# Performance work log

Measured on AMD Instinct MI355X. Metric: run time of the kernel, lower is better.

Reference implementation:

```python
import jax, jax.numpy as jnp
import numpy as np

B, N, RBF, F = 4, 512, 32, 16
EPS = 1e-7


def _levi_civita():
    e = np.zeros((3, 3, 3), np.float32)
    e[0, 1, 2] = e[1, 2, 0] = e[2, 0, 1] = 1.0
    e[0, 2, 1] = e[2, 1, 0] = e[1, 0, 2] = -1.0
    return jnp.asarray(e)


def setup_inputs() -> dict:
    key = jax.random.key(0)
    ks = jax.random.split(key, 8)
    g = lambda k, s, sc=1.0: jax.random.normal(k, s, dtype=jnp.float32) * sc
    w_sc = RBF ** -0.5
    return dict(
        image=jax.random.uniform(ks[0], (B, N, N, RBF), dtype=jnp.float32),
        vectors=g(ks[1], (B, N, N, 3)),
        feat0=g(ks[2], (B, N, F, 1)),
        feat1=g(ks[3], (B, N, F, 3)),
        W00=g(ks[4], (RBF, F), w_sc), b00=jnp.zeros((F,), jnp.float32),
        W01=g(ks[5], (RBF, F), w_sc), b01=jnp.zeros((F,), jnp.float32),
        W10=g(ks[6], (RBF, F), w_sc), b10=jnp.zeros((F,), jnp.float32),
        W11=g(ks[7], (RBF, F), w_sc), b11=jnp.zeros((F,), jnp.float32),
    )


def _masked(radial, vectors):
    # zero the radial where the pair vector has (near) zero norm (self-pairs)
    keep = jnp.linalg.norm(vectors, axis=-1) >= EPS  # (B,N,N)
    return jnp.where(keep[..., None], radial, jnp.zeros_like(radial))


def reference(image, vectors, feat0, feat1, W00, b00, W01, b01, W10, b10, W11, b11):
    # radial networks: Dense(rbf -> F), one per (input tensor, filter order)
    r00 = image @ W00 + b00                      # (B,N,N,F) RO0 filter for RO0 input
    r01 = _masked(image @ W01 + b01, vectors)    # RO1 filter for RO0 input
    r10 = image @ W10 + b10                      # RO0 filter for RO1 input
    r11 = _masked(image @ W11 + b11, vectors)    # RO1 filter for RO1 input

    f0 = feat0[..., 0]                           # (B,N,F)
    # Note: RO1 filter F1[m,a,b,f,j] = vectors[m,a,b,j] * masked_radial[m,a,b,f];
    # fused into the einsums to avoid materializing (B,N,N,F,3).
    out1 = jnp.einsum('mabf,mbf->maf', r00, f0)[..., None]                 # 0x0->0
    out2 = jnp.einsum('mabi,mabf,mbf->mafi', vectors, r01, f0)             # 1x0->1
    out3 = jnp.einsum('mabf,mbfi->mafi', r10, feat1)                       # 0x1->1
    out4 = jnp.einsum('mabj,mabf,mbfj->maf', vectors, r11, feat1)[..., None]  # 1x1->0
    e = _levi_civita()
    out5 = jnp.einsum('ijk,mabj,mabf,mbfk->mafi', e, vectors, r11, feat1)  # 1x1->1
    return (out1, out2, out3, out4, out5)
```

## Files before the change

### kernel.cpp

```cpp
#include <hip/hip_runtime.h>


typedef __attribute__((ext_vector_type(8))) short short8;
typedef __attribute__((ext_vector_type(4))) float f32x4;

#define EPS2 1e-14f

static __device__ __forceinline__ short f2bf(float x) {
    unsigned int u = __float_as_uint(x);
    unsigned int r = (u + 0x7FFFu + ((u >> 16) & 1u)) >> 16;
    return (short)r;
}

__global__ __launch_bounds__(256, 4) void conv_mfma_kernel(
    const float* __restrict__ image,
    const float* __restrict__ vectors,
    const float* __restrict__ feat0,
    const float* __restrict__ feat1,
    const float* __restrict__ W00, const float* __restrict__ b00,
    const float* __restrict__ W01, const float* __restrict__ b01,
    const float* __restrict__ W10, const float* __restrict__ b10,
    const float* __restrict__ W11, const float* __restrict__ b11,
    float* __restrict__ out)
{
    __shared__ float red[4][16][12];

    const int t    = threadIdx.x;
    const int wave = t >> 6;
    const int lane = t & 63;
    const int f    = lane & 15;
    const int g    = lane >> 4;
    const int ma   = blockIdx.x;
    const int m    = ma >> 9;

    short8 wf0, wf1, wf2, wf3;
    float bias0, bias1, bias2, bias3;
    {
        #pragma unroll
        for (int j = 0; j < 8; ++j) {
            const int k = g * 8 + j;
            wf0[j] = f2bf(W00[k * 16 + f]);
            wf1[j] = f2bf(W01[k * 16 + f]);
            wf2[j] = f2bf(W10[k * 16 + f]);
            wf3[j] = f2bf(W11[k * 16 + f]);
        }
        bias0 = b00[f]; bias1 = b01[f]; bias2 = b10[f]; bias3 = b11[f];
    }

    const float* imgbase = image   + (size_t)ma * (512 * 32);
    const float* vecbase = vectors + (size_t)ma * (512 * 3);
    const float* f0base  = feat0   + (size_t)m  * (512 * 16);
    const float* f1base  = feat1   + (size_t)m  * (512 * 16 * 3);

    float acc1 = 0.f, acc4 = 0.f;
    float acc2x = 0.f, acc2y = 0.f, acc2z = 0.f;
    float acc3x = 0.f, acc3y = 0.f, acc3z = 0.f;
    float acc5x = 0.f, acc5y = 0.f, acc5z = 0.f;

    for (int tt = 0; tt < 8; ++tt) {
        const int b0 = wave * 128 + tt * 16;

        const float* arow = imgbase + (size_t)(b0 + f) * 32 + g * 8;
        const float4 a0 = *(const float4*)(arow);
        const float4 a1 = *(const float4*)(arow + 4);
        short8 af;
        af[0] = f2bf(a0.x); af[1] = f2bf(a0.y);
        af[2] = f2bf(a0.z); af[3] = f2bf(a0.w);
        af[4] = f2bf(a1.x); af[5] = f2bf(a1.y);
        af[6] = f2bf(a1.z); af[7] = f2bf(a1.w);

        f32x4 d0 = {0.f, 0.f, 0.f, 0.f};
        f32x4 d1 = {0.f, 0.f, 0.f, 0.f};
        f32x4 d2 = {0.f, 0.f, 0.f, 0.f};
        f32x4 d3 = {0.f, 0.f, 0.f, 0.f};
        d0 = __builtin_amdgcn_mfma_f32_16x16x32_bf16(af, wf0, d0, 0, 0, 0);
        d1 = __builtin_amdgcn_mfma_f32_16x16x32_bf16(af, wf1, d1, 0, 0, 0);
        d2 = __builtin_amdgcn_mfma_f32_16x16x32_bf16(af, wf2, d2, 0, 0, 0);
        d3 = __builtin_amdgcn_mfma_f32_16x16x32_bf16(af, wf3, d3, 0, 0, 0);

        #pragma unroll
        for (int reg = 0; reg < 4; ++reg) {
            const int b = b0 + 4 * g + reg;

            const float* vp = vecbase + b * 3;
            const float vx = vp[0], vy = vp[1], vz = vp[2];
            const float n2 = vx * vx + vy * vy + vz * vz;
            const bool keep = n2 >= EPS2;

            const float f0v = f0base[b * 16 + f];
            const float* f1p = f1base + (size_t)(b * 16 + f) * 3;
            const float u0 = f1p[0], u1 = f1p[1], u2 = f1p[2];

            const float r00 = d0[reg] + bias0;
            const float r01 = keep ? (d1[reg] + bias1) : 0.f;
            const float r10 = d2[reg] + bias2;
            const float r11 = keep ? (d3[reg] + bias3) : 0.f;

            acc1 = fmaf(r00, f0v, acc1);
            const float t01 = r01 * f0v;
            acc2x = fmaf(t01, vx, acc2x);
            acc2y = fmaf(t01, vy, acc2y);
            acc2z = fmaf(t01, vz, acc2z);
            acc3x = fmaf(r10, u0, acc3x);
            acc3y = fmaf(r10, u1, acc3y);
            acc3z = fmaf(r10, u2, acc3z);
            const float d = fmaf(vx, u0, fmaf(vy, u1, vz * u2));
            acc4 = fmaf(r11, d, acc4);
            const float c0 = vy * u2 - vz * u1;
            const float c1 = vz * u0 - vx * u2;
            const float c2 = vx * u1 - vy * u0;
            acc5x = fmaf(r11, c0, acc5x);
            acc5y = fmaf(r11, c1, acc5y);
            acc5z = fmaf(r11, c2, acc5z);
        }
    }

    #define WRED(x) x += __shfl_xor(x, 16); x += __shfl_xor(x, 32);
    WRED(acc1)  WRED(acc2x) WRED(acc2y) WRED(acc2z)
    WRED(acc3x) WRED(acc3y) WRED(acc3z) WRED(acc4)
    WRED(acc5x) WRED(acc5y) WRED(acc5z)
    #undef WRED

    if (lane < 16) {
        red[wave][f][0]  = acc1;
        red[wave][f][1]  = acc2x;
        red[wave][f][2]  = acc2y;
        red[wave][f][3]  = acc2z;
        red[wave][f][4]  = acc3x;
        red[wave][f][5]  = acc3y;
        red[wave][f][6]  = acc3z;
        red[wave][f][7]  = acc4;
        red[wave][f][8]  = acc5x;
        red[wave][f][9]  = acc5y;
        red[wave][f][10] = acc5z;
    }
    __syncthreads();

    if (t < 176) {
        const int ff = t / 11;
        const int comp = t % 11;
        float s = red[0][ff][comp] + red[1][ff][comp]
                + red[2][ff][comp] + red[3][ff][comp];

        const size_t base16 = (size_t)ma * 16 + ff;
        const size_t base48 = base16 * 3;
        if (comp == 0)      out[base16] = s;
        else if (comp < 4)  out[32768  + base48 + (comp - 1)] = s;
        else if (comp < 7)  out[131072 + base48 + (comp - 4)] = s;
        else if (comp == 7) out[229376 + base16] = s;
        else                out[262144 + base48 + (comp - 8)] = s;
    }
}

extern "C" void kernel_launch(void* const* d_in, const int* in_sizes, int n_in,
                              void* d_out, int out_size, void* d_ws, size_t ws_size,
                              hipStream_t stream) {
    const float* image   = (const float*)d_in[0];
    const float* vectors = (const float*)d_in[1];
    const float* feat0   = (const float*)d_in[2];
    const float* feat1   = (const float*)d_in[3];
    const float* W00 = (const float*)d_in[4];
    const float* b00 = (const float*)d_in[5];
    const float* W01 = (const float*)d_in[6];
    const float* b01 = (const float*)d_in[7];
    const float* W10 = (const float*)d_in[8];
    const float* b10 = (const float*)d_in[9];
    const float* W11 = (const float*)d_in[10];
    const float* b11 = (const float*)d_in[11];
    float* out = (float*)d_out;

    conv_mfma_kernel<<<4 * 512, 256, 0, stream>>>(
        image, vectors, feat0, feat1,
        W00, b00, W01, b01, W10, b10, W11, b11, out);
}
```

Baseline: 237.5 us.

## Double-buffer image, vector and feature loads across unrolled tiles

Unrolls the 8-tile loop by hand and keeps two register banks of prefetched image rows, pair vectors and feat0/feat1 values. The loads for the next tile are issued before the MFMA and tail math of the current tile, to hide global-memory latency. Vector loads are widened to three float4 per group of four pairs. The launch bound is lowered to 3 waves per SIMD so the extra live registers fit, at the cost of occupancy.

```diff
diff --git a/kernel.cpp b/kernel.cpp
--- a/kernel.cpp
+++ b/kernel.cpp
@@ -12,7 +12,7 @@
     return (short)r;
 }
 
-__global__ __launch_bounds__(256, 4) void conv_mfma_kernel(
+__global__ __launch_bounds__(256, 3) void conv_mfma_pipe2_kernel(
     const float* __restrict__ image,
     const float* __restrict__ vectors,
     const float* __restrict__ feat0,
@@ -57,63 +57,101 @@
     float acc3x = 0.f, acc3y = 0.f, acc3z = 0.f;
     float acc5x = 0.f, acc5y = 0.f, acc5z = 0.f;
 
-    for (int tt = 0; tt < 8; ++tt) {
-        const int b0 = wave * 128 + tt * 16;
-
-        const float* arow = imgbase + (size_t)(b0 + f) * 32 + g * 8;
-        const float4 a0 = *(const float4*)(arow);
-        const float4 a1 = *(const float4*)(arow + 4);
-        short8 af;
-        af[0] = f2bf(a0.x); af[1] = f2bf(a0.y);
-        af[2] = f2bf(a0.z); af[3] = f2bf(a0.w);
-        af[4] = f2bf(a1.x); af[5] = f2bf(a1.y);
-        af[6] = f2bf(a1.z); af[7] = f2bf(a1.w);
-
-        f32x4 d0 = {0.f, 0.f, 0.f, 0.f};
-        f32x4 d1 = {0.f, 0.f, 0.f, 0.f};
-        f32x4 d2 = {0.f, 0.f, 0.f, 0.f};
-        f32x4 d3 = {0.f, 0.f, 0.f, 0.f};
-        d0 = __builtin_amdgcn_mfma_f32_16x16x32_bf16(af, wf0, d0, 0, 0, 0);
-        d1 = __builtin_amdgcn_mfma_f32_16x16x32_bf16(af, wf1, d1, 0, 0, 0);
-        d2 = __builtin_amdgcn_mfma_f32_16x16x32_bf16(af, wf2, d2, 0, 0, 0);
-        d3 = __builtin_amdgcn_mfma_f32_16x16x32_bf16(af, wf3, d3, 0, 0, 0);
-
-        #pragma unroll
-        for (int reg = 0; reg < 4; ++reg) {
-            const int b = b0 + 4 * g + reg;
-
-            const float* vp = vecbase + b * 3;
-            const float vx = vp[0], vy = vp[1], vz = vp[2];
-            const float n2 = vx * vx + vy * vy + vz * vz;
-            const bool keep = n2 >= EPS2;
-
-            const float f0v = f0base[b * 16 + f];
-            const float* f1p = f1base + (size_t)(b * 16 + f) * 3;
-            const float u0 = f1p[0], u1 = f1p[1], u2 = f1p[2];
-
-            const float r00 = d0[reg] + bias0;
-            const float r01 = keep ? (d1[reg] + bias1) : 0.f;
-            const float r10 = d2[reg] + bias2;
-            const float r11 = keep ? (d3[reg] + bias3) : 0.f;
-
-            acc1 = fmaf(r00, f0v, acc1);
-            const float t01 = r01 * f0v;
-            acc2x = fmaf(t01, vx, acc2x);
-            acc2y = fmaf(t01, vy, acc2y);
-            acc2z = fmaf(t01, vz, acc2z);
-            acc3x = fmaf(r10, u0, acc3x);
-            acc3y = fmaf(r10, u1, acc3y);
-            acc3z = fmaf(r10, u2, acc3z);
-            const float d = fmaf(vx, u0, fmaf(vy, u1, vz * u2));
-            acc4 = fmaf(r11, d, acc4);
-            const float c0 = vy * u2 - vz * u1;
-            const float c1 = vz * u0 - vx * u2;
-            const float c2 = vx * u1 - vy * u0;
-            acc5x = fmaf(r11, c0, acc5x);
-            acc5y = fmaf(r11, c1, acc5y);
-            acc5z = fmaf(r11, c2, acc5z);
-        }
-    }
+    const int bbase = wave * 128;
+
+#define DECL_BANK(S) \
+    float4 A0##S, A1##S, V0##S, V1##S, V2##S; \
+    float F0a##S, F0b##S, F0c##S, F0d##S; \
+    float P00##S, P01##S, P02##S, P10##S, P11##S, P12##S; \
+    float P20##S, P21##S, P22##S, P30##S, P31##S, P32##S;
+
+#define LOAD_BANK(S, B0) { \
+    const float* arow_ = imgbase + (size_t)((B0) + f) * 32 + g * 8; \
+    A0##S = *(const float4*)(arow_); \
+    A1##S = *(const float4*)(arow_ + 4); \
+    const int bb_ = (B0) + 4 * g; \
+    const float* vp_ = vecbase + bb_ * 3; \
+    V0##S = *(const float4*)(vp_); \
+    V1##S = *(const float4*)(vp_ + 4); \
+    V2##S = *(const float4*)(vp_ + 8); \
+    const float* f0p_ = f0base + bb_ * 16 + f; \
+    F0a##S = f0p_[0]; F0b##S = f0p_[16]; F0c##S = f0p_[32]; F0d##S = f0p_[48]; \
+    const float* f1p_ = f1base + (size_t)(bb_ * 16 + f) * 3; \
+    P00##S = f1p_[0];   P01##S = f1p_[1];   P02##S = f1p_[2]; \
+    P10##S = f1p_[48];  P11##S = f1p_[49];  P12##S = f1p_[50]; \
+    P20##S = f1p_[96];  P21##S = f1p_[97];  P22##S = f1p_[98]; \
+    P30##S = f1p_[144]; P31##S = f1p_[145]; P32##S = f1p_[146]; \
+}
+
+#define TAIL(R00, R01, R10, R11, VX, VY, VZ, F0V, U0, U1, U2) { \
+    const float vx_ = (VX), vy_ = (VY), vz_ = (VZ); \
+    const float n2_ = vx_ * vx_ + vy_ * vy_ + vz_ * vz_; \
+    const bool keep_ = n2_ >= EPS2; \
+    const float r00_ = (R00) + bias0; \
+    const float r01_ = keep_ ? ((R01) + bias1) : 0.f; \
+    const float r10_ = (R10) + bias2; \
+    const float r11_ = keep_ ? ((R11) + bias3) : 0.f; \
+    const float f0v_ = (F0V); \
+    const float u0_ = (U0), u1_ = (U1), u2_ = (U2); \
+    acc1 = fmaf(r00_, f0v_, acc1); \
+    const float t01_ = r01_ * f0v_; \
+    acc2x = fmaf(t01_, vx_, acc2x); \
+    acc2y = fmaf(t01_, vy_, acc2y); \
+    acc2z = fmaf(t01_, vz_, acc2z); \
+    acc3x = fmaf(r10_, u0_, acc3x); \
+    acc3y = fmaf(r10_, u1_, acc3y); \
+    acc3z = fmaf(r10_, u2_, acc3z); \
+    const float dd_ = fmaf(vx_, u0_, fmaf(vy_, u1_, vz_ * u2_)); \
+    acc4 = fmaf(r11_, dd_, acc4); \
+    acc5x = fmaf(r11_, vy_ * u2_ - vz_ * u1_, acc5x); \
+    acc5y = fmaf(r11_, vz_ * u0_ - vx_ * u2_, acc5y); \
+    acc5z = fmaf(r11_, vx_ * u1_ - vy_ * u0_, acc5z); \
+}
+
+#define COMPUTE_BANK(S) { \
+    short8 af_; \
+    af_[0] = f2bf(A0##S.x); af_[1] = f2bf(A0##S.y); \
+    af_[2] = f2bf(A0##S.z); af_[3] = f2bf(A0##S.w); \
+    af_[4] = f2bf(A1##S.x); af_[5] = f2bf(A1##S.y); \
+    af_[6] = f2bf(A1##S.z); af_[7] = f2bf(A1##S.w); \
+    f32x4 d0_ = {0.f, 0.f, 0.f, 0.f}; \
+    f32x4 d1_ = {0.f, 0.f, 0.f, 0.f}; \
+    f32x4 d2_ = {0.f, 0.f, 0.f, 0.f}; \
+    f32x4 d3_ = {0.f, 0.f, 0.f, 0.f}; \
+    d0_ = __builtin_amdgcn_mfma_f32_16x16x32_bf16(af_, wf0, d0_, 0, 0, 0); \
+    d1_ = __builtin_amdgcn_mfma_f32_16x16x32_bf16(af_, wf1, d1_, 0, 0, 0); \
+    d2_ = __builtin_amdgcn_mfma_f32_16x16x32_bf16(af_, wf2, d2_, 0, 0, 0); \
+    d3_ = __builtin_amdgcn_mfma_f32_16x16x32_bf16(af_, wf3, d3_, 0, 0, 0); \
+    TAIL(d0_[0], d1_[0], d2_[0], d3_[0], V0##S.x, V0##S.y, V0##S.z, F0a##S, P00##S, P01##S, P02##S) \
+    TAIL(d0_[1], d1_[1], d2_[1], d3_[1], V0##S.w, V1##S.x, V1##S.y, F0b##S, P10##S, P11##S, P12##S) \
+    TAIL(d0_[2], d1_[2], d2_[2], d3_[2], V1##S.z, V1##S.w, V2##S.x, F0c##S, P20##S, P21##S, P22##S) \
+    TAIL(d0_[3], d1_[3], d2_[3], d3_[3], V2##S.y, V2##S.z, V2##S.w, F0d##S, P30##S, P31##S, P32##S) \
+}
+
+    DECL_BANK(A)
+    DECL_BANK(B)
+
+    LOAD_BANK(A, bbase +   0)
+    LOAD_BANK(B, bbase +  16)
+    COMPUTE_BANK(A)
+    LOAD_BANK(A, bbase +  32)
+    COMPUTE_BANK(B)
+    LOAD_BANK(B, bbase +  48)
+    COMPUTE_BANK(A)
+    LOAD_BANK(A, bbase +  64)
+    COMPUTE_BANK(B)
+    LOAD_BANK(B, bbase +  80)
+    COMPUTE_BANK(A)
+    LOAD_BANK(A, bbase +  96)
+    COMPUTE_BANK(B)
+    LOAD_BANK(B, bbase + 112)
+    COMPUTE_BANK(A)
+    COMPUTE_BANK(B)
+
+#undef DECL_BANK
+#undef LOAD_BANK
+#undef TAIL
+#undef COMPUTE_BANK
 
     #define WRED(x) x += __shfl_xor(x, 16); x += __shfl_xor(x, 32);
     WRED(acc1)  WRED(acc2x) WRED(acc2y) WRED(acc2z)
@@ -169,7 +207,7 @@
     const float* b11 = (const float*)d_in[11];
     float* out = (float*)d_out;
 
-    conv_mfma_kernel<<<4 * 512, 256, 0, stream>>>(
+    conv_mfma_pipe2_kernel<<<4 * 512, 256, 0, stream>>>(
         image, vectors, feat0, feat1,
         W00, b00, W01, b01, W10, b10, W11, b11, out);
 }
```

New measurement: 303.9 us. 1.28x slower.
